# Kernel tuning notes

Measured on AMD Instinct MI355X. Metric: run time of the kernel, lower is better.

Reference implementation:

```python
import jax, jax.numpy as jnp
import numpy as np

N_NODES = 100_000
N_EDGES = 3_200_000
F_IN, HID, OUT = 64, 64, 6


def setup_inputs() -> dict:
    key = jax.random.key(0)
    k1, k2, k3, k4 = jax.random.split(key, 4)
    x = jax.random.normal(k1, (N_NODES, F_IN), dtype=jnp.float32)
    edge_index = jax.random.randint(k2, (2, N_EDGES), 0, N_NODES, dtype=jnp.int32)
    W1 = jax.random.normal(k3, (F_IN, HID), dtype=jnp.float32) * (1.0 / np.sqrt(F_IN))
    b1 = jnp.zeros((HID,), dtype=jnp.float32)
    W2 = jax.random.normal(k4, (HID, OUT), dtype=jnp.float32) * (1.0 / np.sqrt(HID))
    b2 = jnp.zeros((OUT,), dtype=jnp.float32)
    return {"x": x, "edge_index": edge_index, "W1": W1, "b1": b1, "W2": W2, "b2": b2}


def _gcn_conv(x, row, col, norm, W, b):
    # x: [N, F_in], row/col/norm: [E'], W: [F_in, F_out]
    n = x.shape[0]
    h = x @ W                                   # [N, F_out]
    msg = h[row] * norm[:, None]                # gather + scale, [E', F_out]
    out = jax.ops.segment_sum(msg, col, num_segments=n)  # scatter-add to targets
    return out + b


def reference(x, edge_index, W1, b1, W2, b2):
    n = x.shape[0]
    # add self-loops (PyG GCNConv default)
    loops = jnp.arange(n, dtype=edge_index.dtype)
    row = jnp.concatenate([edge_index[0], loops])  # source
    col = jnp.concatenate([edge_index[1], loops])  # target
    # symmetric normalization: deg computed at target incl. self-loops
    deg = jax.ops.segment_sum(jnp.ones_like(col, dtype=x.dtype), col, num_segments=n)
    dinv = jnp.where(deg > 0, jax.lax.rsqrt(deg), 0.0)
    norm = dinv[row] * dinv[col]                # [E']

    h = jax.nn.relu(_gcn_conv(x, row, col, norm, W1, b1))
    out = _gcn_conv(h, row, col, norm, W2, b2)
    return jnp.mean(out, axis=0)                # [OUT]
```

## Files before the change

### kernel.cpp

```cpp
#include <hip/hip_runtime.h>

#define N_NODES 100000
#define N_EDGES 3200000
#define NOUT 6

#define NPB 256
#define NBUK ((N_NODES + NPB - 1) / NPB)
#define CAP 12288
#define PCHUNK 4096
#define PNB ((N_EDGES + PCHUNK - 1) / PCHUNK)
#define SORT_CAP 10240
#define AGB (N_NODES / 32)
#define NPART (2 * AGB)

typedef __attribute__((ext_vector_type(2))) float v2f;

__global__ __launch_bounds__(512) void k_initcur(int* __restrict__ gcursor) {
    int t = threadIdx.x;
    if (t < NBUK) gcursor[t] = 0;
}

__global__ __launch_bounds__(512) void k_partition(const int* __restrict__ row,
                                                   const int* __restrict__ col,
                                                   int* __restrict__ gcursor,
                                                   int* __restrict__ bedge) {
    __shared__ int hist[512];
    __shared__ int lstart[512];
    __shared__ int lcur[512];
    __shared__ int gbase[512];
    __shared__ int sscan[512];
    __shared__ int stage[PCHUNK];
    __shared__ unsigned short stageb[PCHUNK];

    const int t = threadIdx.x;
    const int c0 = blockIdx.x * PCHUNK;
    int cnt = N_EDGES - c0; if (cnt > PCHUNK) cnt = PCHUNK;

    hist[t] = 0; lcur[t] = 0;
    __syncthreads();

    int myp[8]; int myb[8];
#pragma unroll
    for (int i = 0; i < 8; ++i) {
        int p = i * 512 + t;
        myb[i] = -1;
        if (p < cnt) {
            int e = c0 + p;
            int c = col[e], r = row[e];
            int b = c >> 8;
            myp[i] = ((c & 255) << 17) | r;
            myb[i] = b;
            atomicAdd(&hist[b], 1);
        }
    }
    __syncthreads();

    int hv = hist[t];
    sscan[t] = hv;
    __syncthreads();
    for (int off = 1; off < 512; off <<= 1) {
        int u = (t >= off) ? sscan[t - off] : 0;
        __syncthreads();
        sscan[t] += u;
        __syncthreads();
    }
    lstart[t] = sscan[t] - hv;
    if (t < NBUK && hv > 0) gbase[t] = atomicAdd(&gcursor[t], hv);
    __syncthreads();

#pragma unroll
    for (int i = 0; i < 8; ++i) {
        if (myb[i] >= 0) {
            int pos = lstart[myb[i]] + atomicAdd(&lcur[myb[i]], 1);
            stage[pos] = myp[i];
            stageb[pos] = (unsigned short)myb[i];
        }
    }
    __syncthreads();

    for (int p = t; p < cnt; p += 512) {
        int b = stageb[p];
        int rel = gbase[b] + p - lstart[b];
        if (rel < CAP) bedge[b * CAP + rel] = stage[p];
    }
}

__global__ __launch_bounds__(512) void k_bucket_sort(const int* __restrict__ gcursor,
                                                     const int* __restrict__ bedge,
                                                     float* __restrict__ dinv,
                                                     int* __restrict__ node_off,
                                                     int* __restrict__ sorted_row) {
    __shared__ int cnt[NPB];
    __shared__ int lstart[NPB];
    __shared__ int lcur[NPB];
    __shared__ int sc[NPB];
    __shared__ int stage[SORT_CAP];

    const int t = threadIdx.x;
    const int b = blockIdx.x;
    const int s = b * CAP;
    int m = gcursor[b]; if (m > CAP) m = CAP;
    const bool fits = (m <= SORT_CAP);

    if (t < NPB) { cnt[t] = 0; lcur[t] = 0; }
    __syncthreads();

    if (fits) {
        for (int j = t; j < m; j += 512) {
            int p = bedge[s + j];
            stage[j] = p;
            atomicAdd(&cnt[p >> 17], 1);
        }
    } else {
        for (int j = t; j < m; j += 512) atomicAdd(&cnt[bedge[s + j] >> 17], 1);
    }
    __syncthreads();

    if (t < NPB) sc[t] = cnt[t];
    __syncthreads();
    for (int off = 1; off < NPB; off <<= 1) {
        int u = 0;
        if (t < NPB && t >= off) u = sc[t - off];
        __syncthreads();
        if (t < NPB && t >= off) sc[t] += u;
        __syncthreads();
    }
    if (t < NPB) {
        int c = cnt[t];
        lstart[t] = sc[t] - c;
        node_off[b * 257 + t] = s + sc[t] - c;
        int g = b * NPB + t;
        if (g < N_NODES) dinv[g] = rsqrtf((float)c + 1.0f);
    }
    if (t == 256) node_off[b * 257 + 256] = s + m;
    __syncthreads();

    if (fits) {
        for (int j = t; j < m; j += 512) {
            int p = stage[j];
            int lc = p >> 17;
            int pos = lstart[lc] + atomicAdd(&lcur[lc], 1);
            sorted_row[s + pos] = p & 0x1FFFF;
        }
    } else {
        for (int j = t; j < m; j += 512) {
            int p = bedge[s + j];
            int lc = p >> 17;
            int pos = lstart[lc] + atomicAdd(&lcur[lc], 1);
            sorted_row[s + pos] = p & 0x1FFFF;
        }
    }
}

__global__ __launch_bounds__(256) void k_gemm1(const float* __restrict__ x,
                                               const float* __restrict__ W1,
                                               const float* __restrict__ dinv,
                                               unsigned int* __restrict__ hs1b) {
    __shared__ float Ws[64 * 64];
    __shared__ float Xs[64 * 65];
    const int tx = threadIdx.x;
    const int nodeBase = blockIdx.x * 64;

    for (int t = tx; t < 64 * 64; t += 256) Ws[t] = W1[t];

    for (int t = tx; t < 64 * 16; t += 256) {
        int r = t >> 4, c4 = t & 15;
        int g = nodeBase + r;
        float4 v = make_float4(0.f, 0.f, 0.f, 0.f);
        if (g < N_NODES) v = reinterpret_cast<const float4*>(x)[g * 16 + c4];
        float* p = &Xs[r * 65 + c4 * 4];
        p[0] = v.x; p[1] = v.y; p[2] = v.z; p[3] = v.w;
    }
    __syncthreads();

    const int nG = tx >> 4;
    const int cG = tx & 15;
    float acc[4][4] = {};
    for (int k = 0; k < 64; ++k) {
        float4 w = *reinterpret_cast<const float4*>(&Ws[k * 64 + cG * 4]);
#pragma unroll
        for (int i = 0; i < 4; ++i) {
            float xv = Xs[(nG * 4 + i) * 65 + k];
            acc[i][0] = fmaf(xv, w.x, acc[i][0]);
            acc[i][1] = fmaf(xv, w.y, acc[i][1]);
            acc[i][2] = fmaf(xv, w.z, acc[i][2]);
            acc[i][3] = fmaf(xv, w.w, acc[i][3]);
        }
    }

#pragma unroll
    for (int i = 0; i < 4; ++i) {
        int n = nodeBase + nG * 4 + i;
        if (n < N_NODES) {
            float dv = dinv[n];
            int u = __builtin_amdgcn_cvt_pk_fp8_f32(acc[i][0] * dv, acc[i][1] * dv, 0, false);
            u = __builtin_amdgcn_cvt_pk_fp8_f32(acc[i][2] * dv, acc[i][3] * dv, u, true);
            hs1b[n * 16 + cG] = (unsigned int)u;
        }
    }
}

__device__ inline void addrow8(float* __restrict__ acc, uint2 u) {
    v2f p0 = __builtin_amdgcn_cvt_pk_f32_fp8((int)u.x, false);
    v2f p1 = __builtin_amdgcn_cvt_pk_f32_fp8((int)u.x, true);
    v2f p2 = __builtin_amdgcn_cvt_pk_f32_fp8((int)u.y, false);
    v2f p3 = __builtin_amdgcn_cvt_pk_f32_fp8((int)u.y, true);
    acc[0] += p0.x; acc[1] += p0.y; acc[2] += p1.x; acc[3] += p1.y;
    acc[4] += p2.x; acc[5] += p2.y; acc[6] += p3.x; acc[7] += p3.y;
}

__global__ __launch_bounds__(256) void k_agg_l2(const int* __restrict__ node_off,
                                                const int* __restrict__ sorted_row,
                                                const unsigned int* __restrict__ hs1b,
                                                const float* __restrict__ W2,
                                                const float* __restrict__ b1,
                                                const float* __restrict__ dinv,
                                                float* __restrict__ hs2,
                                                float* __restrict__ partials) {
    __shared__ float W2s[64 * NOUT];
    __shared__ float b1s[64];
    __shared__ float pacc[8];
    const int tx = threadIdx.x;
    for (int t = tx; t < 64 * NOUT; t += 256) W2s[t] = W2[t];
    if (tx < 64) b1s[tx] = b1[tx];
    if (tx < 8) pacc[tx] = 0.f;
    __syncthreads();

    const int node = (blockIdx.x * 256 + tx) >> 3;
    const int l = tx & 7;
    const int gb = tx & 56;
    const int idx = (node >> 8) * 257 + (node & 255);
    const int s = node_off[idx], e = node_off[idx + 1];
    const uint2* hsrc = reinterpret_cast<const uint2*>(hs1b);

    float acc[8] = {};
    addrow8(acc, hsrc[node * 8 + l]);
    int j = s;
    const int nb = (e - s) >> 3;
    if (nb >= 2) {
        int idxA = sorted_row[j + l];
        uint2 gv[8];
#pragma unroll
        for (int k = 0; k < 8; ++k) {
            int rk = __shfl(idxA, gb + k, 64);
            gv[k] = hsrc[rk * 8 + l];
        }
        int idxB = sorted_row[j + 8 + l];
        for (int bi = 2; bi < nb; ++bi) {
            int idxC = sorted_row[j + bi * 8 + l];
            uint2 nv[8];
#pragma unroll
            for (int k = 0; k < 8; ++k) {
                int rk = __shfl(idxB, gb + k, 64);
                nv[k] = hsrc[rk * 8 + l];
            }
#pragma unroll
            for (int k = 0; k < 8; ++k) addrow8(acc, gv[k]);
#pragma unroll
            for (int k = 0; k < 8; ++k) gv[k] = nv[k];
            idxB = idxC;
        }
        {
            uint2 nv[8];
#pragma unroll
            for (int k = 0; k < 8; ++k) {
                int rk = __shfl(idxB, gb + k, 64);
                nv[k] = hsrc[rk * 8 + l];
            }
#pragma unroll
            for (int k = 0; k < 8; ++k) addrow8(acc, gv[k]);
#pragma unroll
            for (int k = 0; k < 8; ++k) addrow8(acc, nv[k]);
        }
        j += nb * 8;
    } else if (nb == 1) {
        int idxA = sorted_row[j + l];
        uint2 gv[8];
#pragma unroll
        for (int k = 0; k < 8; ++k) {
            int rk = __shfl(idxA, gb + k, 64);
            gv[k] = hsrc[rk * 8 + l];
        }
#pragma unroll
        for (int k = 0; k < 8; ++k) addrow8(acc, gv[k]);
        j += 8;
    }
    for (; j < e; ++j) addrow8(acc, hsrc[sorted_row[j] * 8 + l]);

    const float dv = dinv[node];
    float sj[NOUT] = {};
#pragma unroll
    for (int i = 0; i < 8; ++i) {
        float hv = fmaxf(fmaf(dv, acc[i], b1s[l * 8 + i]), 0.f);
#pragma unroll
        for (int q = 0; q < NOUT; ++q) sj[q] = fmaf(hv, W2s[(l * 8 + i) * NOUT + q], sj[q]);
    }
#pragma unroll
    for (int q = 0; q < NOUT; ++q) {
        sj[q] += __shfl_xor(sj[q], 1, 64);
        sj[q] += __shfl_xor(sj[q], 2, 64);
        sj[q] += __shfl_xor(sj[q], 4, 64);
    }
    if (l == 0) {
        float4 o0 = make_float4(sj[0] * dv, sj[1] * dv, sj[2] * dv, sj[3] * dv);
        float4 o1 = make_float4(sj[4] * dv, sj[5] * dv, 0.f, 0.f);
        reinterpret_cast<float4*>(hs2)[node * 2] = o0;
        reinterpret_cast<float4*>(hs2)[node * 2 + 1] = o1;
        float sc = dv * dv;
#pragma unroll
        for (int q = 0; q < NOUT; ++q) atomicAdd(&pacc[q], sj[q] * sc);
    }
    __syncthreads();
    if (tx < NOUT) partials[blockIdx.x * 8 + tx] = pacc[tx];
}

__global__ __launch_bounds__(256) void k_wsum2(const int* __restrict__ node_off,
                                               const int* __restrict__ sorted_row,
                                               const float* __restrict__ dinv,
                                               const float* __restrict__ hs2,
                                               float* __restrict__ partials) {
    const int tx = threadIdx.x;
    const int node = (blockIdx.x * 256 + tx) >> 3;
    const int l = tx & 7;
    const int gb = tx & 56;
    const int idx = (node >> 8) * 257 + (node & 255);
    const int s = node_off[idx], e = node_off[idx + 1];

    float a = 0.f;
    int j = s;
    const int nb = (e - s) >> 3;
    if (nb >= 2) {
        int idxA = sorted_row[j + l];
        float gv[8];
#pragma unroll
        for (int k = 0; k < 8; ++k) {
            int rk = __shfl(idxA, gb + k, 64);
            gv[k] = hs2[rk * 8 + l];
        }
        int idxB = sorted_row[j + 8 + l];
        for (int bi = 2; bi < nb; ++bi) {
            int idxC = sorted_row[j + bi * 8 + l];
            float nv[8];
#pragma unroll
            for (int k = 0; k < 8; ++k) {
                int rk = __shfl(idxB, gb + k, 64);
                nv[k] = hs2[rk * 8 + l];
            }
            a += ((gv[0] + gv[1]) + (gv[2] + gv[3])) + ((gv[4] + gv[5]) + (gv[6] + gv[7]));
#pragma unroll
            for (int k = 0; k < 8; ++k) gv[k] = nv[k];
            idxB = idxC;
        }
        {
            float nv[8];
#pragma unroll
            for (int k = 0; k < 8; ++k) {
                int rk = __shfl(idxB, gb + k, 64);
                nv[k] = hs2[rk * 8 + l];
            }
            a += ((gv[0] + gv[1]) + (gv[2] + gv[3])) + ((gv[4] + gv[5]) + (gv[6] + gv[7]));
            a += ((nv[0] + nv[1]) + (nv[2] + nv[3])) + ((nv[4] + nv[5]) + (nv[6] + nv[7]));
        }
        j += nb * 8;
    } else if (nb == 1) {
        int idxA = sorted_row[j + l];
#pragma unroll
        for (int k = 0; k < 8; ++k) {
            int rk = __shfl(idxA, gb + k, 64);
            a += hs2[rk * 8 + l];
        }
        j += 8;
    }
    for (; j < e; ++j) a += hs2[sorted_row[j] * 8 + l];
    a *= dinv[node];

    a += __shfl_xor(a, 8, 64);
    a += __shfl_xor(a, 16, 64);
    a += __shfl_xor(a, 32, 64);
    __shared__ float wred[4][8];
    const int lane = tx & 63, w = tx >> 6;
    if (lane < 8) wred[w][lane] = a;
    __syncthreads();
    if (tx < 8)
        partials[(AGB + blockIdx.x) * 8 + tx] = wred[0][tx] + wred[1][tx] + wred[2][tx] + wred[3][tx];
}

__global__ __launch_bounds__(256) void k_reduce2(const float* __restrict__ partials,
                                                 const float* __restrict__ b2,
                                                 float* __restrict__ out) {
    __shared__ float s[256];
    for (int j = 0; j < NOUT; ++j) {
        float a = 0.f;
        for (int p = threadIdx.x; p < NPART; p += 256) a += partials[p * 8 + j];
        s[threadIdx.x] = a;
        __syncthreads();
        for (int off = 128; off > 0; off >>= 1) {
            if (threadIdx.x < off) s[threadIdx.x] += s[threadIdx.x + off];
            __syncthreads();
        }
        if (threadIdx.x == 0) out[j] = b2[j] + s[0] * (1.0f / N_NODES);
        __syncthreads();
    }
}

extern "C" void kernel_launch(void* const* d_in, const int* in_sizes, int n_in,
                              void* d_out, int out_size, void* d_ws, size_t ws_size,
                              hipStream_t stream) {
    const float* x  = (const float*)d_in[0];
    const int*   ei = (const int*)d_in[1];
    const float* W1 = (const float*)d_in[2];
    const float* b1 = (const float*)d_in[3];
    const float* W2 = (const float*)d_in[4];
    const float* b2 = (const float*)d_in[5];
    float* out = (float*)d_out;

    unsigned int* hs1b = (unsigned int*)d_ws;
    float* dinv      = (float*)(hs1b + 1600000);
    float* hs2       = dinv + 100352;
    float* partials  = hs2 + 800000;
    int*   gcursor   = (int*)(partials + 50176);
    int*   node_off  = gcursor + 512;
    int*   sorted_row= node_off + 100864;
    int*   bedge     = sorted_row + 4804608;

    const int* row = ei;
    const int* col = ei + N_EDGES;

    k_initcur<<<1, 512, 0, stream>>>(gcursor);
    k_partition<<<PNB, 512, 0, stream>>>(row, col, gcursor, bedge);
    k_bucket_sort<<<NBUK, 512, 0, stream>>>(gcursor, bedge, dinv, node_off, sorted_row);

    k_gemm1<<<(N_NODES + 63) / 64, 256, 0, stream>>>(x, W1, dinv, hs1b);

    k_agg_l2<<<AGB, 256, 0, stream>>>(node_off, sorted_row, hs1b, W2, b1, dinv, hs2, partials);

    k_wsum2<<<AGB, 256, 0, stream>>>(node_off, sorted_row, dinv, hs2, partials);

    k_reduce2<<<1, 256, 0, stream>>>(partials, b2, out);
}
```

Before: 177.5 us.

## Compute final weighted sum directly from bucketed edge list instead of CSR

Replaces the per-node CSR gather kernel for the last weighted sum with a kernel that walks the bucket-partitioned packed edge list (target-local index in high bits, source in low bits). Each bucket is split across two blocks, dinv for the bucket is staged in shared memory, and contributions are accumulated with fmaf without per-node segmentation. This removes the CSR offset lookups and irregular per-node loop lengths, at the cost of relying on the packed bedge encoding and CAP clamp. Also replaces the cursor-init kernel with a hipMemsetAsync.

```diff
diff --git a/kernel.cpp b/kernel.cpp
--- a/kernel.cpp
+++ b/kernel.cpp
@@ -11,14 +11,10 @@
 #define PNB ((N_EDGES + PCHUNK - 1) / PCHUNK)
 #define SORT_CAP 10240
 #define AGB (N_NODES / 32)
-#define NPART (2 * AGB)
+#define WSB (2 * NBUK)
+#define NPART (AGB + WSB)
 
 typedef __attribute__((ext_vector_type(2))) float v2f;
-
-__global__ __launch_bounds__(512) void k_initcur(int* __restrict__ gcursor) {
-    int t = threadIdx.x;
-    if (t < NBUK) gcursor[t] = 0;
-}
 
 __global__ __launch_bounds__(512) void k_partition(const int* __restrict__ row,
                                                    const int* __restrict__ col,
@@ -314,75 +310,54 @@
     if (tx < NOUT) partials[blockIdx.x * 8 + tx] = pacc[tx];
 }
 
-__global__ __launch_bounds__(256) void k_wsum2(const int* __restrict__ node_off,
-                                               const int* __restrict__ sorted_row,
+__global__ __launch_bounds__(512) void k_wsumb(const int* __restrict__ gcursor,
+                                               const int* __restrict__ bedge,
                                                const float* __restrict__ dinv,
                                                const float* __restrict__ hs2,
                                                float* __restrict__ partials) {
-    const int tx = threadIdx.x;
-    const int node = (blockIdx.x * 256 + tx) >> 3;
-    const int l = tx & 7;
-    const int gb = tx & 56;
-    const int idx = (node >> 8) * 257 + (node & 255);
-    const int s = node_off[idx], e = node_off[idx + 1];
+    __shared__ float ddv[NPB];
+    __shared__ float wred[8][8];
+    const int t = threadIdx.x;
+    const int b = blockIdx.x >> 1;
+    const int h = blockIdx.x & 1;
+    if (t < NPB) {
+        int g = b * NPB + t;
+        ddv[t] = (g < N_NODES) ? dinv[g] : 0.f;
+    }
+    __syncthreads();
+
+    int m = gcursor[b]; if (m > CAP) m = CAP;
+    const int js = (m >> 1) & ~0; const int lo = h ? js : 0; const int hi = h ? m : js;
+    const int* src = bedge + b * CAP;
+    const int l = t & 7, g = t >> 3;
 
     float a = 0.f;
-    int j = s;
-    const int nb = (e - s) >> 3;
-    if (nb >= 2) {
-        int idxA = sorted_row[j + l];
-        float gv[8];
-#pragma unroll
-        for (int k = 0; k < 8; ++k) {
-            int rk = __shfl(idxA, gb + k, 64);
-            gv[k] = hs2[rk * 8 + l];
-        }
-        int idxB = sorted_row[j + 8 + l];
-        for (int bi = 2; bi < nb; ++bi) {
-            int idxC = sorted_row[j + bi * 8 + l];
-            float nv[8];
-#pragma unroll
-            for (int k = 0; k < 8; ++k) {
-                int rk = __shfl(idxB, gb + k, 64);
-                nv[k] = hs2[rk * 8 + l];
-            }
-            a += ((gv[0] + gv[1]) + (gv[2] + gv[3])) + ((gv[4] + gv[5]) + (gv[6] + gv[7]));
-#pragma unroll
-            for (int k = 0; k < 8; ++k) gv[k] = nv[k];
-            idxB = idxC;
-        }
-        {
-            float nv[8];
-#pragma unroll
-            for (int k = 0; k < 8; ++k) {
-                int rk = __shfl(idxB, gb + k, 64);
-                nv[k] = hs2[rk * 8 + l];
-            }
-            a += ((gv[0] + gv[1]) + (gv[2] + gv[3])) + ((gv[4] + gv[5]) + (gv[6] + gv[7]));
-            a += ((nv[0] + nv[1]) + (nv[2] + nv[3])) + ((nv[4] + nv[5]) + (nv[6] + nv[7]));
-        }
-        j += nb * 8;
-    } else if (nb == 1) {
-        int idxA = sorted_row[j + l];
-#pragma unroll
-        for (int k = 0; k < 8; ++k) {
-            int rk = __shfl(idxA, gb + k, 64);
-            a += hs2[rk * 8 + l];
-        }
-        j += 8;
-    }
-    for (; j < e; ++j) a += hs2[sorted_row[j] * 8 + l];
-    a *= dinv[node];
+    int j = lo + g;
+    for (; j + 64 < hi; j += 128) {
+        int p0 = src[j];
+        int p1 = src[j + 64];
+        float v0 = hs2[(p0 & 0x1FFFF) * 8 + l];
+        float v1 = hs2[(p1 & 0x1FFFF) * 8 + l];
+        a = fmaf(ddv[p0 >> 17], v0, a);
+        a = fmaf(ddv[p1 >> 17], v1, a);
+    }
+    if (j < hi) {
+        int p0 = src[j];
+        a = fmaf(ddv[p0 >> 17], hs2[(p0 & 0x1FFFF) * 8 + l], a);
+    }
 
     a += __shfl_xor(a, 8, 64);
     a += __shfl_xor(a, 16, 64);
     a += __shfl_xor(a, 32, 64);
-    __shared__ float wred[4][8];
-    const int lane = tx & 63, w = tx >> 6;
+    const int lane = t & 63, w = t >> 6;
     if (lane < 8) wred[w][lane] = a;
     __syncthreads();
-    if (tx < 8)
-        partials[(AGB + blockIdx.x) * 8 + tx] = wred[0][tx] + wred[1][tx] + wred[2][tx] + wred[3][tx];
+    if (t < 8) {
+        float s = 0.f;
+#pragma unroll
+        for (int ww = 0; ww < 8; ++ww) s += wred[ww][t];
+        partials[(AGB + blockIdx.x) * 8 + t] = s;
+    }
 }
 
 __global__ __launch_bounds__(256) void k_reduce2(const float* __restrict__ partials,
@@ -426,7 +401,7 @@
     const int* row = ei;
     const int* col = ei + N_EDGES;
 
-    k_initcur<<<1, 512, 0, stream>>>(gcursor);
+    hipMemsetAsync(gcursor, 0, NBUK * sizeof(int), stream);
     k_partition<<<PNB, 512, 0, stream>>>(row, col, gcursor, bedge);
     k_bucket_sort<<<NBUK, 512, 0, stream>>>(gcursor, bedge, dinv, node_off, sorted_row);
 
@@ -434,7 +409,7 @@
 
     k_agg_l2<<<AGB, 256, 0, stream>>>(node_off, sorted_row, hs1b, W2, b1, dinv, hs2, partials);
 
-    k_wsum2<<<AGB, 256, 0, stream>>>(node_off, sorted_row, dinv, hs2, partials);
+    k_wsumb<<<WSB, 512, 0, stream>>>(gcursor, bedge, dinv, hs2, partials);
 
     k_reduce2<<<1, 256, 0, stream>>>(partials, b2, out);
 }
```

New measurement: 171.5 us. 3.4% less time.
